# Kernel optimization log

Measured on AMD Instinct MI355X. Metric: run time of the kernel, lower is better.

## Reference

```python
import jax, jax.numpy as jnp
import numpy as np

N = 8192


def setup_inputs() -> dict:
    key = jax.random.key(0)
    ks = jax.random.split(key, 12)
    H_emb = jax.random.normal(ks[0], (645, 1140), jnp.float32) * 0.05
    H_emb = H_emb.at[0].set(0.0)  # padding_idx=0
    inp = {
        "ld_gcn": jax.random.normal(ks[1], (N, 512), jnp.float32),
        "ld_encoder": jax.random.normal(ks[2], (N, 512), jnp.float32),
        "x": jax.random.randint(ks[3], (N,), 0, 240),
        "y": jax.random.randint(ks[4], (N,), 0, 404),
        "H_emb": H_emb,
        "conv_w": jax.random.normal(ks[5], (32, 1, 2, 25), jnp.float32) * (1.0 / np.sqrt(2 * 25)),
        "conv_b": jnp.zeros((32,), jnp.float32),
        "W1": jax.random.normal(ks[6], (1000, 3968), jnp.float32) * (1.0 / np.sqrt(3968)),
        "b1": jnp.zeros((1000,), jnp.float32),
        "W2": jax.random.normal(ks[7], (100, 1000), jnp.float32) * (1.0 / np.sqrt(1000)),
        "b2": jnp.zeros((100,), jnp.float32),
        "Wg": jax.random.normal(ks[8], (100, 512), jnp.float32) * (1.0 / np.sqrt(512)),
        "bg": jnp.zeros((100,), jnp.float32),
        "We": jax.random.normal(ks[9], (100, 512), jnp.float32) * (1.0 / np.sqrt(512)),
        "be": jnp.zeros((100,), jnp.float32),
    }
    return inp


def reference(ld_gcn, ld_encoder, x, y, H_emb, conv_w, conv_b, W1, b1, W2, b2, Wg, bg, We, be):
    n = x.shape[0]
    lrelu = lambda t: jax.nn.leaky_relu(t, 0.01)
    # embedding lookups + concat -> (n,1,2,1140)
    h = jnp.concatenate([H_emb[x], H_emb[y + 240]], axis=1).reshape(n, 1, 2, 1140)
    # CNN: conv (2,25) stride (1,9) valid -> (n,32,1,124)
    c = jax.lax.conv_general_dilated(h, conv_w, window_strides=(1, 9), padding="VALID",
                                     dimension_numbers=("NCHW", "OIHW", "NCHW"))
    c = lrelu(c + conv_b[None, :, None, None]).reshape(n, -1)  # (n,3968)
    # fc_H (dropout = identity at eval)
    hfc = lrelu(c @ W1.T + b1)
    hfc = lrelu(hfc @ W2.T + b2)  # (n,100)
    # gating projections
    g = jnp.tanh(ld_gcn @ Wg.T + bg)       # (n,100)
    e = jnp.tanh(ld_encoder @ We.T + be)   # (n,100)
    # diagonal of (n,100)@(100,n) == row-wise dot product
    a_gcn = jnp.einsum("nd,nd->n", g, hfc)
    a_enc = jnp.einsum("nd,nd->n", e, hfc)
    att = jax.nn.softmax(jnp.stack([a_gcn, a_enc], axis=1), axis=1)  # (n,2)
    return ld_gcn * att[:, :1], ld_encoder * att[:, 1:]
```

## Files before the change

### kernel.cpp

```cpp
#include <hip/hip_runtime.h>
#include <hip/hip_bf16.h>

typedef unsigned short u16;
typedef short bf16x8 __attribute__((ext_vector_type(8)));
typedef float f32x4 __attribute__((ext_vector_type(4)));

#define NROWS 8192
#define EMBD  1140
#define FDIM  3968
#define N1R   1000
#define N1P   1024
#define N2R   100
#define N2P   128
#define DG    512

__device__ inline u16 f2b(float f) {
  __hip_bfloat16 h = __float2bfloat16(f);
  return *reinterpret_cast<u16*>(&h);
}

__device__ inline float b2f(u16 u) {
  unsigned v = (unsigned)u << 16;
  union { unsigned u; float f; } c;
  c.u = v;
  return c.f;
}

__device__ inline float tanh_fast(float x) {
  float ax = fabsf(x);
  float t = __expf(-2.f * ax);
  float r = (1.f - t) / (1.f + t);
  return x < 0.f ? -r : r;
}

__device__ inline void gld16(const void* g, void* l) {
  __builtin_amdgcn_global_load_lds(
      (const __attribute__((address_space(1))) unsigned int*)g,
      (__attribute__((address_space(3))) unsigned int*)l, 16, 0, 0);
}

__global__ __launch_bounds__(256) void prep_kernel(
    const float* __restrict__ W1, const float* __restrict__ W2,
    const float* __restrict__ Wg, const float* __restrict__ We,
    const float* __restrict__ H_emb, const float* __restrict__ conv_w,
    const float* __restrict__ conv_b,
    u16* __restrict__ W1bf, u16* __restrict__ W2bf,
    u16* __restrict__ Wgbf, u16* __restrict__ Webf,
    u16* __restrict__ Abuf, u16* __restrict__ Bbuf) {
  const int b = blockIdx.x;
  const int t = threadIdx.x;
  if (b < 2112) {
    const float* src;
    u16* dst;
    int row, c8, realRow, realCol;
    if (b < 1984) {
      int id = b * 256 + t;
      row = id / 496; c8 = (id - row * 496) * 8;
      src = W1 + (size_t)row * FDIM + c8;
      dst = W1bf + (size_t)row * FDIM + c8;
      realRow = N1R; realCol = FDIM;
    } else if (b < 2048) {
      int id = (b - 1984) * 256 + t;
      row = id >> 7; c8 = (id & 127) * 8;
      src = W2 + (size_t)row * N1R + c8;
      dst = W2bf + (size_t)row * N1P + c8;
      realRow = N2R; realCol = N1R;
    } else if (b < 2080) {
      int id = (b - 2048) * 256 + t;
      row = id >> 6; c8 = (id & 63) * 8;
      src = Wg + (size_t)row * DG + c8;
      dst = Wgbf + (size_t)row * DG + c8;
      realRow = N2R; realCol = DG;
    } else {
      int id = (b - 2080) * 256 + t;
      row = id >> 6; c8 = (id & 63) * 8;
      src = We + (size_t)row * DG + c8;
      dst = Webf + (size_t)row * DG + c8;
      realRow = N2R; realCol = DG;
    }
    bf16x8 o = (bf16x8){0, 0, 0, 0, 0, 0, 0, 0};
    if (row < realRow && c8 < realCol) {
#pragma unroll
      for (int j = 0; j < 8; ++j) o[j] = (short)f2b(src[j]);
    }
    *(bf16x8*)dst = o;
    return;
  }
  __shared__ float se[EMBD];
  __shared__ float sw[32 * 25];
  __shared__ float sb[32];
  const int eb = b - 2112;
  bool isA = eb < 240;
  const float* emb = H_emb + (size_t)eb * EMBD;
  u16* outp = isA ? (Abuf + (size_t)eb * FDIM) : (Bbuf + (size_t)(eb - 240) * FDIM);
  for (int i = t; i < EMBD; i += 256) se[i] = emb[i];
  int kh = isA ? 0 : 1;
  for (int i = t; i < 800; i += 256) {
    int o = i / 25, kw = i - o * 25;
    sw[i] = conv_w[o * 50 + kh * 25 + kw];
  }
  if (t < 32) sb[t] = isA ? conv_b[t] : 0.f;
  __syncthreads();
  for (int f = t; f < FDIM; f += 256) {
    int o = f / 124, wpos = f - o * 124;
    const float* e = se + wpos * 9;
    const float* wp = sw + o * 25;
    float acc = sb[o];
#pragma unroll
    for (int kw = 0; kw < 25; ++kw) acc += wp[kw] * e[kw];
    outp[f] = f2b(acc);
  }
}

__global__ __launch_bounds__(256) void conv_combine_kernel(
    const u16* __restrict__ Abuf, const u16* __restrict__ Bbuf,
    const int* __restrict__ xi, const int* __restrict__ yi, u16* __restrict__ cbf) {
  int r = blockIdx.x;
  const bf16x8* pa = (const bf16x8*)(Abuf + (size_t)xi[r] * FDIM);
  const bf16x8* pb = (const bf16x8*)(Bbuf + (size_t)yi[r] * FDIM);
  bf16x8* out = (bf16x8*)(cbf + (size_t)r * FDIM);
  for (int i = threadIdx.x; i < FDIM / 8; i += 256) {
    bf16x8 a = pa[i], b = pb[i];
    bf16x8 o;
#pragma unroll
    for (int j = 0; j < 8; ++j) {
      float v = b2f((u16)a[j]) + b2f((u16)b[j]);
      v = v > 0.f ? v : 0.01f * v;
      o[j] = (short)f2b(v);
    }
    out[i] = o;
  }
}

__global__ __launch_bounds__(256) void fc1_kernel(
    const u16* __restrict__ A, const u16* __restrict__ B,
    const float* __restrict__ bias, int realN,
    u16* __restrict__ C, int K, int ldc, int nTilesX) {
  const int nwg = gridDim.x;
  const int cpx = nwg >> 3;
  const int bid = blockIdx.x;
  const int wg = (bid & 7) * cpx + (bid >> 3);
  const int tm = (wg / nTilesX) * 128;
  const int tn = (wg % nTilesX) * 128;

  __shared__ u16 As[2][8192];
  __shared__ u16 Bs[2][8192];
  const int t = threadIdx.x;
  const int lane = t & 63;
  const int w = t >> 6;
  const int wr = (w >> 1) * 64, wc = (w & 1) * 64;
  const int fr = lane & 15;
  const int kg = lane >> 4;

  const int srow = lane >> 3;
  const int su = ((lane & 7) ^ srow) * 8;
  const u16* gA[4];
  const u16* gB[4];
  int ldsOff[4];
#pragma unroll
  for (int i = 0; i < 4; ++i) {
    const int c = w + i * 4;
    gA[i] = A + (size_t)(tm + c * 8 + srow) * K + su;
    gB[i] = B + (size_t)(tn + c * 8 + srow) * K + su;
    ldsOff[i] = c * 512;
  }

  f32x4 acc[4][4];
#pragma unroll
  for (int m = 0; m < 4; ++m)
#pragma unroll
    for (int n = 0; n < 4; ++n) acc[m][n] = (f32x4){0.f, 0.f, 0.f, 0.f};

  const int nk = K >> 6;
#pragma unroll
  for (int i = 0; i < 4; ++i) {
    gld16(gA[i], &As[0][ldsOff[i]]);
    gld16(gB[i], &Bs[0][ldsOff[i]]);
  }
  __syncthreads();

  for (int kt = 0; kt < nk; ++kt) {
    const int cb = kt & 1;
    if (kt + 1 < nk) {
      const int ko = (kt + 1) << 6;
#pragma unroll
      for (int i = 0; i < 4; ++i) {
        gld16(gA[i] + ko, &As[cb ^ 1][ldsOff[i]]);
        gld16(gB[i] + ko, &Bs[cb ^ 1][ldsOff[i]]);
      }
    }
    __builtin_amdgcn_sched_barrier(0);
#pragma unroll
    for (int ks = 0; ks < 2; ++ks) {
      const int un = ((ks * 4 + kg) ^ (fr & 7)) << 4;
      bf16x8 af[4], bff[4];
#pragma unroll
      for (int m = 0; m < 4; ++m)
        af[m] = *(const bf16x8*)((const char*)As[cb] + (wr + m * 16 + fr) * 128 + un);
#pragma unroll
      for (int n = 0; n < 4; ++n)
        bff[n] = *(const bf16x8*)((const char*)Bs[cb] + (wc + n * 16 + fr) * 128 + un);
#pragma unroll
      for (int m = 0; m < 4; ++m)
#pragma unroll
        for (int n = 0; n < 4; ++n)
          acc[m][n] = __builtin_amdgcn_mfma_f32_16x16x32_bf16(af[m], bff[n], acc[m][n], 0, 0, 0);
    }
    __syncthreads();
  }

#pragma unroll
  for (int n = 0; n < 4; ++n) {
    int col = tn + wc + n * 16 + fr;
    float bv = (col < realN) ? bias[col] : 0.f;
#pragma unroll
    for (int m = 0; m < 4; ++m) {
#pragma unroll
      for (int j = 0; j < 4; ++j) {
        int row = tm + wr + m * 16 + kg * 4 + j;
        float v = acc[m][n][j] + bv;
        v = v > 0.f ? v : 0.01f * v;
        C[(size_t)row * ldc + col] = f2b(v);
      }
    }
  }
}

__global__ __launch_bounds__(256) void tail_kernel(
    const u16* __restrict__ hfc1, const u16* __restrict__ W2bf, const float* __restrict__ b2,
    const float* __restrict__ ldg, const float* __restrict__ lde,
    const u16* __restrict__ Wgbf, const float* __restrict__ bg,
    const u16* __restrict__ Webf, const float* __restrict__ be,
    float* __restrict__ out0, float* __restrict__ out1) {
  __shared__ float H16[N2P][16];
  __shared__ float dpart[2][4][16];
  __shared__ float wt[2][16];

  const int tm = blockIdx.x * 16;
  const int t = threadIdx.x;
  const int lane = t & 63;
  const int w = t >> 6;
  const int fr = lane & 15;
  const int kg = lane >> 4;
  const int n0 = w * 2;

  {
    f32x4 a0e = (f32x4){0.f, 0.f, 0.f, 0.f}, a0o = a0e, a1e = a0e, a1o = a0e;
    const u16* Ap = hfc1 + (size_t)(tm + fr) * N1P + kg * 8;
    const u16* B0 = W2bf + (size_t)(n0 * 16 + fr) * N1P + kg * 8;
    const u16* B1 = B0 + (size_t)16 * N1P;
#pragma unroll 4
    for (int k2 = 0; k2 < 16; ++k2) {
      bf16x8 afe = *(const bf16x8*)(Ap + k2 * 64);
      bf16x8 afo = *(const bf16x8*)(Ap + k2 * 64 + 32);
      bf16x8 f0e = *(const bf16x8*)(B0 + k2 * 64);
      bf16x8 f0o = *(const bf16x8*)(B0 + k2 * 64 + 32);
      bf16x8 f1e = *(const bf16x8*)(B1 + k2 * 64);
      bf16x8 f1o = *(const bf16x8*)(B1 + k2 * 64 + 32);
      a0e = __builtin_amdgcn_mfma_f32_16x16x32_bf16(afe, f0e, a0e, 0, 0, 0);
      a1e = __builtin_amdgcn_mfma_f32_16x16x32_bf16(afe, f1e, a1e, 0, 0, 0);
      a0o = __builtin_amdgcn_mfma_f32_16x16x32_bf16(afo, f0o, a0o, 0, 0, 0);
      a1o = __builtin_amdgcn_mfma_f32_16x16x32_bf16(afo, f1o, a1o, 0, 0, 0);
    }
#pragma unroll
    for (int n = 0; n < 2; ++n) {
      int col = (n0 + n) * 16 + fr;
      float bv = (col < N2R) ? b2[col] : 0.f;
      f32x4 o;
#pragma unroll
      for (int j = 0; j < 4; ++j) {
        float x = (n == 0 ? a0e[j] + a0o[j] : a1e[j] + a1o[j]) + bv;
        o[j] = x > 0.f ? x : 0.01f * x;
      }
      *(f32x4*)&H16[col][kg * 4] = o;
    }
  }
  __syncthreads();

#pragma unroll 1
  for (int sec = 0; sec < 2; ++sec) {
    const float* ld = sec == 0 ? ldg : lde;
    const u16* Wb = sec == 0 ? Wgbf : Webf;
    const float* bb = sec == 0 ? bg : be;

    f32x4 a0e = (f32x4){0.f, 0.f, 0.f, 0.f}, a0o = a0e, a1e = a0e, a1o = a0e;
    const float* Ap = ld + (size_t)(tm + fr) * DG + kg * 8;
    const u16* B0 = Wb + (size_t)(n0 * 16 + fr) * DG + kg * 8;
    const u16* B1 = B0 + (size_t)16 * DG;
#pragma unroll 2
    for (int k2 = 0; k2 < 8; ++k2) {
      float4 v0 = *(const float4*)(Ap + k2 * 64);
      float4 v1 = *(const float4*)(Ap + k2 * 64 + 4);
      float4 v2 = *(const float4*)(Ap + k2 * 64 + 32);
      float4 v3 = *(const float4*)(Ap + k2 * 64 + 36);
      bf16x8 afe, afo;
      afe[0] = (short)f2b(v0.x); afe[1] = (short)f2b(v0.y);
      afe[2] = (short)f2b(v0.z); afe[3] = (short)f2b(v0.w);
      afe[4] = (short)f2b(v1.x); afe[5] = (short)f2b(v1.y);
      afe[6] = (short)f2b(v1.z); afe[7] = (short)f2b(v1.w);
      afo[0] = (short)f2b(v2.x); afo[1] = (short)f2b(v2.y);
      afo[2] = (short)f2b(v2.z); afo[3] = (short)f2b(v2.w);
      afo[4] = (short)f2b(v3.x); afo[5] = (short)f2b(v3.y);
      afo[6] = (short)f2b(v3.z); afo[7] = (short)f2b(v3.w);
      bf16x8 f0e = *(const bf16x8*)(B0 + k2 * 64);
      bf16x8 f0o = *(const bf16x8*)(B0 + k2 * 64 + 32);
      bf16x8 f1e = *(const bf16x8*)(B1 + k2 * 64);
      bf16x8 f1o = *(const bf16x8*)(B1 + k2 * 64 + 32);
      a0e = __builtin_amdgcn_mfma_f32_16x16x32_bf16(afe, f0e, a0e, 0, 0, 0);
      a1e = __builtin_amdgcn_mfma_f32_16x16x32_bf16(afe, f1e, a1e, 0, 0, 0);
      a0o = __builtin_amdgcn_mfma_f32_16x16x32_bf16(afo, f0o, a0o, 0, 0, 0);
      a1o = __builtin_amdgcn_mfma_f32_16x16x32_bf16(afo, f1o, a1o, 0, 0, 0);
    }
    float dv[4] = {0.f, 0.f, 0.f, 0.f};
#pragma unroll
    for (int n = 0; n < 2; ++n) {
      int col = (n0 + n) * 16 + fr;
      float bv = (col < N2R) ? bb[col] : 0.f;
      f32x4 h = *(const f32x4*)&H16[col][kg * 4];
#pragma unroll
      for (int j = 0; j < 4; ++j) {
        float s = (n == 0 ? a0e[j] + a0o[j] : a1e[j] + a1o[j]) + bv;
        dv[j] += tanh_fast(s) * h[j];
      }
    }
#pragma unroll
    for (int j = 0; j < 4; ++j) {
      float v = dv[j];
      v += __shfl_xor(v, 1);
      v += __shfl_xor(v, 2);
      v += __shfl_xor(v, 4);
      v += __shfl_xor(v, 8);
      dv[j] = v;
    }
    if (fr == 0) {
#pragma unroll
      for (int j = 0; j < 4; ++j) dpart[sec][w][kg * 4 + j] = dv[j];
    }
  }
  __syncthreads();

  if (t < 16) {
    float ag = dpart[0][0][t] + dpart[0][1][t] + dpart[0][2][t] + dpart[0][3][t];
    float ae = dpart[1][0][t] + dpart[1][1][t] + dpart[1][2][t] + dpart[1][3][t];
    float mm = fmaxf(ag, ae);
    float eg = __expf(ag - mm), eo = __expf(ae - mm);
    float inv = 1.f / (eg + eo);
    wt[0][t] = eg * inv;
    wt[1][t] = eo * inv;
  }
  __syncthreads();

  for (int i = t; i < 16 * (DG / 4); i += 256) {
    int r = i >> 7, c = i & 127;
    float w0 = wt[0][r], w1 = wt[1][r];
    size_t off = (size_t)(tm + r) * DG + c * 4;
    float4 a = *(const float4*)(ldg + off);
    a.x *= w0; a.y *= w0; a.z *= w0; a.w *= w0;
    *(float4*)(out0 + off) = a;
    float4 b = *(const float4*)(lde + off);
    b.x *= w1; b.y *= w1; b.z *= w1; b.w *= w1;
    *(float4*)(out1 + off) = b;
  }
}

extern "C" void kernel_launch(void* const* d_in, const int* in_sizes, int n_in,
                              void* d_out, int out_size, void* d_ws, size_t ws_size,
                              hipStream_t stream) {
  const float* ld_gcn = (const float*)d_in[0];
  const float* ld_enc = (const float*)d_in[1];
  const int*   xi     = (const int*)d_in[2];
  const int*   yi     = (const int*)d_in[3];
  const float* H_emb  = (const float*)d_in[4];
  const float* conv_w = (const float*)d_in[5];
  const float* conv_b = (const float*)d_in[6];
  const float* W1     = (const float*)d_in[7];
  const float* b1     = (const float*)d_in[8];
  const float* W2     = (const float*)d_in[9];
  const float* b2     = (const float*)d_in[10];
  const float* Wg     = (const float*)d_in[11];
  const float* bg     = (const float*)d_in[12];
  const float* We     = (const float*)d_in[13];
  const float* be     = (const float*)d_in[14];

  char* ws = (char*)d_ws;
  size_t off = 0;
  auto alloc = [&](size_t bytes) -> void* {
    void* p = ws + off;
    off = (off + bytes + 255) & ~(size_t)255;
    return p;
  };
  u16* Abuf = (u16*)alloc(240ull * FDIM * 2);
  u16* Bbuf = (u16*)alloc(404ull * FDIM * 2);
  u16* cbf  = (u16*)alloc((size_t)NROWS * FDIM * 2);
  u16* W1bf = (u16*)alloc((size_t)N1P * FDIM * 2);
  u16* W2bf = (u16*)alloc((size_t)N2P * N1P * 2);
  u16* Wgbf = (u16*)alloc((size_t)N2P * DG * 2);
  u16* Webf = (u16*)alloc((size_t)N2P * DG * 2);
  u16* hfc1 = (u16*)alloc((size_t)NROWS * N1P * 2);
  if (ws_size < off) return;

  prep_kernel<<<2756, 256, 0, stream>>>(W1, W2, Wg, We, H_emb, conv_w, conv_b,
                                        W1bf, W2bf, Wgbf, Webf, Abuf, Bbuf);
  conv_combine_kernel<<<NROWS, 256, 0, stream>>>(Abuf, Bbuf, xi, yi, cbf);

  fc1_kernel<<<dim3((NROWS / 128) * (N1P / 128)), 256, 0, stream>>>(
      cbf, W1bf, b1, N1R, hfc1, FDIM, N1P, N1P / 128);

  float* out0 = (float*)d_out;
  float* out1 = out0 + (size_t)NROWS * DG;
  tail_kernel<<<NROWS / 16, 256, 0, stream>>>(
      hfc1, W2bf, b2, ld_gcn, ld_enc, Wgbf, bg, Webf, be, out0, out1);
}
```

Baseline: 184.2 us.

## Move gating projections into gather kernel and precompute tanh outputs

```diff
diff --git a/kernel.cpp b/kernel.cpp
--- a/kernel.cpp
+++ b/kernel.cpp
@@ -33,6 +33,15 @@
   return x < 0.f ? -r : r;
 }
 
+__device__ inline bf16x8 cvt8(float4 a, float4 b) {
+  bf16x8 o;
+  o[0] = (short)f2b(a.x); o[1] = (short)f2b(a.y);
+  o[2] = (short)f2b(a.z); o[3] = (short)f2b(a.w);
+  o[4] = (short)f2b(b.x); o[5] = (short)f2b(b.y);
+  o[6] = (short)f2b(b.z); o[7] = (short)f2b(b.w);
+  return o;
+}
+
 __device__ inline void gld16(const void* g, void* l) {
   __builtin_amdgcn_global_load_lds(
       (const __attribute__((address_space(1))) unsigned int*)g,
@@ -41,15 +50,13 @@
 
 __global__ __launch_bounds__(256) void prep_kernel(
     const float* __restrict__ W1, const float* __restrict__ W2,
-    const float* __restrict__ Wg, const float* __restrict__ We,
     const float* __restrict__ H_emb, const float* __restrict__ conv_w,
     const float* __restrict__ conv_b,
     u16* __restrict__ W1bf, u16* __restrict__ W2bf,
-    u16* __restrict__ Wgbf, u16* __restrict__ Webf,
     u16* __restrict__ Abuf, u16* __restrict__ Bbuf) {
   const int b = blockIdx.x;
   const int t = threadIdx.x;
-  if (b < 2112) {
+  if (b < 2048) {
     const float* src;
     u16* dst;
     int row, c8, realRow, realCol;
@@ -59,24 +66,12 @@
       src = W1 + (size_t)row * FDIM + c8;
       dst = W1bf + (size_t)row * FDIM + c8;
       realRow = N1R; realCol = FDIM;
-    } else if (b < 2048) {
+    } else {
       int id = (b - 1984) * 256 + t;
       row = id >> 7; c8 = (id & 127) * 8;
       src = W2 + (size_t)row * N1R + c8;
       dst = W2bf + (size_t)row * N1P + c8;
       realRow = N2R; realCol = N1R;
-    } else if (b < 2080) {
-      int id = (b - 2048) * 256 + t;
-      row = id >> 6; c8 = (id & 63) * 8;
-      src = Wg + (size_t)row * DG + c8;
-      dst = Wgbf + (size_t)row * DG + c8;
-      realRow = N2R; realCol = DG;
-    } else {
-      int id = (b - 2080) * 256 + t;
-      row = id >> 6; c8 = (id & 63) * 8;
-      src = We + (size_t)row * DG + c8;
-      dst = Webf + (size_t)row * DG + c8;
-      realRow = N2R; realCol = DG;
     }
     bf16x8 o = (bf16x8){0, 0, 0, 0, 0, 0, 0, 0};
     if (row < realRow && c8 < realCol) {
@@ -89,7 +84,7 @@
   __shared__ float se[EMBD];
   __shared__ float sw[32 * 25];
   __shared__ float sb[32];
-  const int eb = b - 2112;
+  const int eb = b - 2048;
   bool isA = eb < 240;
   const float* emb = H_emb + (size_t)eb * EMBD;
   u16* outp = isA ? (Abuf + (size_t)eb * FDIM) : (Bbuf + (size_t)(eb - 240) * FDIM);
@@ -112,23 +107,91 @@
   }
 }
 
-__global__ __launch_bounds__(256) void conv_combine_kernel(
+__global__ __launch_bounds__(256) void cc_kernel(
     const u16* __restrict__ Abuf, const u16* __restrict__ Bbuf,
-    const int* __restrict__ xi, const int* __restrict__ yi, u16* __restrict__ cbf) {
-  int r = blockIdx.x;
-  const bf16x8* pa = (const bf16x8*)(Abuf + (size_t)xi[r] * FDIM);
-  const bf16x8* pb = (const bf16x8*)(Bbuf + (size_t)yi[r] * FDIM);
-  bf16x8* out = (bf16x8*)(cbf + (size_t)r * FDIM);
-  for (int i = threadIdx.x; i < FDIM / 8; i += 256) {
-    bf16x8 a = pa[i], b = pb[i];
-    bf16x8 o;
-#pragma unroll
-    for (int j = 0; j < 8; ++j) {
-      float v = b2f((u16)a[j]) + b2f((u16)b[j]);
-      v = v > 0.f ? v : 0.01f * v;
-      o[j] = (short)f2b(v);
-    }
-    out[i] = o;
+    const int* __restrict__ xi, const int* __restrict__ yi, u16* __restrict__ cbf,
+    const float* __restrict__ ldg, const float* __restrict__ lde,
+    const float* __restrict__ Wg, const float* __restrict__ We,
+    const float* __restrict__ bg, const float* __restrict__ be,
+    float* __restrict__ G, float* __restrict__ E) {
+  const int b = blockIdx.x;
+  const int t = threadIdx.x;
+  if (b < NROWS) {
+    const bf16x8* pa = (const bf16x8*)(Abuf + (size_t)xi[b] * FDIM);
+    const bf16x8* pb = (const bf16x8*)(Bbuf + (size_t)yi[b] * FDIM);
+    bf16x8* out = (bf16x8*)(cbf + (size_t)b * FDIM);
+    for (int i = t; i < FDIM / 8; i += 256) {
+      bf16x8 a = pa[i], bb = pb[i];
+      bf16x8 o;
+#pragma unroll
+      for (int j = 0; j < 8; ++j) {
+        float v = b2f((u16)a[j]) + b2f((u16)bb[j]);
+        v = v > 0.f ? v : 0.01f * v;
+        o[j] = (short)f2b(v);
+      }
+      out[i] = o;
+    }
+    return;
+  }
+  __shared__ float sH[16][128];
+  const int eb = b - NROWS;
+  const int sec = eb >> 9;
+  const int tm = (eb & 511) * 16;
+  const float* ld = sec ? lde : ldg;
+  const float* Wraw = sec ? We : Wg;
+  const float* bb = sec ? be : bg;
+  float* Gout = sec ? E : G;
+
+  const int lane = t & 63;
+  const int w = t >> 6;
+  const int fr = lane & 15;
+  const int kg = lane >> 4;
+  const int n0 = w * 2;
+
+  f32x4 a0e = (f32x4){0.f, 0.f, 0.f, 0.f}, a0o = a0e, a1e = a0e, a1o = a0e;
+  const float* Ap = ld + (size_t)(tm + fr) * DG + kg * 8;
+  const int r0 = n0 * 16 + fr, r1 = r0 + 16;
+  const bool val0 = r0 < N2R, val1 = r1 < N2R;
+  const float* W0 = Wraw + (size_t)(val0 ? r0 : 0) * DG + kg * 8;
+  const float* W1p = Wraw + (size_t)(val1 ? r1 : 0) * DG + kg * 8;
+  const bf16x8 z8 = (bf16x8){0, 0, 0, 0, 0, 0, 0, 0};
+#pragma unroll 2
+  for (int k2 = 0; k2 < 8; ++k2) {
+    float4 v0 = *(const float4*)(Ap + k2 * 64);
+    float4 v1 = *(const float4*)(Ap + k2 * 64 + 4);
+    float4 v2 = *(const float4*)(Ap + k2 * 64 + 32);
+    float4 v3 = *(const float4*)(Ap + k2 * 64 + 36);
+    bf16x8 afe = cvt8(v0, v1), afo = cvt8(v2, v3);
+    bf16x8 f0e = z8, f0o = z8, f1e = z8, f1o = z8;
+    if (val0) {
+      f0e = cvt8(*(const float4*)(W0 + k2 * 64), *(const float4*)(W0 + k2 * 64 + 4));
+      f0o = cvt8(*(const float4*)(W0 + k2 * 64 + 32), *(const float4*)(W0 + k2 * 64 + 36));
+    }
+    if (val1) {
+      f1e = cvt8(*(const float4*)(W1p + k2 * 64), *(const float4*)(W1p + k2 * 64 + 4));
+      f1o = cvt8(*(const float4*)(W1p + k2 * 64 + 32), *(const float4*)(W1p + k2 * 64 + 36));
+    }
+    a0e = __builtin_amdgcn_mfma_f32_16x16x32_bf16(afe, f0e, a0e, 0, 0, 0);
+    a1e = __builtin_amdgcn_mfma_f32_16x16x32_bf16(afe, f1e, a1e, 0, 0, 0);
+    a0o = __builtin_amdgcn_mfma_f32_16x16x32_bf16(afo, f0o, a0o, 0, 0, 0);
+    a1o = __builtin_amdgcn_mfma_f32_16x16x32_bf16(afo, f1o, a1o, 0, 0, 0);
+  }
+#pragma unroll
+  for (int n = 0; n < 2; ++n) {
+    int col = (n0 + n) * 16 + fr;
+    float bv = (col < N2R) ? bb[col] : 0.f;
+#pragma unroll
+    for (int j = 0; j < 4; ++j) {
+      float s = (n == 0 ? a0e[j] + a0o[j] : a1e[j] + a1o[j]) + bv;
+      sH[kg * 4 + j][col] = tanh_fast(s);
+    }
+  }
+  __syncthreads();
+  {
+    int row = t >> 4, c0 = (t & 15) * 8;
+    float* dst = Gout + (size_t)(tm + row) * N2P + c0;
+    *(f32x4*)dst = *(const f32x4*)&sH[row][c0];
+    *(f32x4*)(dst + 4) = *(const f32x4*)&sH[row][c0 + 4];
   }
 }
 
@@ -228,12 +291,12 @@
 
 __global__ __launch_bounds__(256) void tail_kernel(
     const u16* __restrict__ hfc1, const u16* __restrict__ W2bf, const float* __restrict__ b2,
+    const float* __restrict__ G, const float* __restrict__ E,
     const float* __restrict__ ldg, const float* __restrict__ lde,
-    const u16* __restrict__ Wgbf, const float* __restrict__ bg,
-    const u16* __restrict__ Webf, const float* __restrict__ be,
     float* __restrict__ out0, float* __restrict__ out1) {
   __shared__ float H16[N2P][16];
-  __shared__ float dpart[2][4][16];
+  __shared__ float dsG[4][16];
+  __shared__ float dsE[4][16];
   __shared__ float wt[2][16];
 
   const int tm = blockIdx.x * 16;
@@ -277,71 +340,27 @@
   }
   __syncthreads();
 
-#pragma unroll 1
-  for (int sec = 0; sec < 2; ++sec) {
-    const float* ld = sec == 0 ? ldg : lde;
-    const u16* Wb = sec == 0 ? Wgbf : Webf;
-    const float* bb = sec == 0 ? bg : be;
-
-    f32x4 a0e = (f32x4){0.f, 0.f, 0.f, 0.f}, a0o = a0e, a1e = a0e, a1o = a0e;
-    const float* Ap = ld + (size_t)(tm + fr) * DG + kg * 8;
-    const u16* B0 = Wb + (size_t)(n0 * 16 + fr) * DG + kg * 8;
-    const u16* B1 = B0 + (size_t)16 * DG;
-#pragma unroll 2
-    for (int k2 = 0; k2 < 8; ++k2) {
-      float4 v0 = *(const float4*)(Ap + k2 * 64);
-      float4 v1 = *(const float4*)(Ap + k2 * 64 + 4);
-      float4 v2 = *(const float4*)(Ap + k2 * 64 + 32);
-      float4 v3 = *(const float4*)(Ap + k2 * 64 + 36);
-      bf16x8 afe, afo;
-      afe[0] = (short)f2b(v0.x); afe[1] = (short)f2b(v0.y);
-      afe[2] = (short)f2b(v0.z); afe[3] = (short)f2b(v0.w);
-      afe[4] = (short)f2b(v1.x); afe[5] = (short)f2b(v1.y);
-      afe[6] = (short)f2b(v1.z); afe[7] = (short)f2b(v1.w);
-      afo[0] = (short)f2b(v2.x); afo[1] = (short)f2b(v2.y);
-      afo[2] = (short)f2b(v2.z); afo[3] = (short)f2b(v2.w);
-      afo[4] = (short)f2b(v3.x); afo[5] = (short)f2b(v3.y);
-      afo[6] = (short)f2b(v3.z); afo[7] = (short)f2b(v3.w);
-      bf16x8 f0e = *(const bf16x8*)(B0 + k2 * 64);
-      bf16x8 f0o = *(const bf16x8*)(B0 + k2 * 64 + 32);
-      bf16x8 f1e = *(const bf16x8*)(B1 + k2 * 64);
-      bf16x8 f1o = *(const bf16x8*)(B1 + k2 * 64 + 32);
-      a0e = __builtin_amdgcn_mfma_f32_16x16x32_bf16(afe, f0e, a0e, 0, 0, 0);
-      a1e = __builtin_amdgcn_mfma_f32_16x16x32_bf16(afe, f1e, a1e, 0, 0, 0);
-      a0o = __builtin_amdgcn_mfma_f32_16x16x32_bf16(afo, f0o, a0o, 0, 0, 0);
-      a1o = __builtin_amdgcn_mfma_f32_16x16x32_bf16(afo, f1o, a1o, 0, 0, 0);
-    }
-    float dv[4] = {0.f, 0.f, 0.f, 0.f};
-#pragma unroll
-    for (int n = 0; n < 2; ++n) {
-      int col = (n0 + n) * 16 + fr;
-      float bv = (col < N2R) ? bb[col] : 0.f;
-      f32x4 h = *(const f32x4*)&H16[col][kg * 4];
-#pragma unroll
-      for (int j = 0; j < 4; ++j) {
-        float s = (n == 0 ? a0e[j] + a0o[j] : a1e[j] + a1o[j]) + bv;
-        dv[j] += tanh_fast(s) * h[j];
-      }
-    }
-#pragma unroll
-    for (int j = 0; j < 4; ++j) {
-      float v = dv[j];
-      v += __shfl_xor(v, 1);
-      v += __shfl_xor(v, 2);
-      v += __shfl_xor(v, 4);
-      v += __shfl_xor(v, 8);
-      dv[j] = v;
-    }
-    if (fr == 0) {
-#pragma unroll
-      for (int j = 0; j < 4; ++j) dpart[sec][w][kg * 4 + j] = dv[j];
-    }
+  {
+    const int drow = t & 15;
+    const int d0 = (t >> 4 & 15) * 8;
+    float pg = 0.f, pe = 0.f;
+    const float* Gp = G + (size_t)(tm + drow) * N2P + d0;
+    const float* Ep = E + (size_t)(tm + drow) * N2P + d0;
+#pragma unroll
+    for (int j = 0; j < 8; ++j) {
+      float h = H16[d0 + j][drow];
+      pg += Gp[j] * h;
+      pe += Ep[j] * h;
+    }
+    pg += __shfl_xor(pg, 16); pg += __shfl_xor(pg, 32);
+    pe += __shfl_xor(pe, 16); pe += __shfl_xor(pe, 32);
+    if (lane < 16) { dsG[w][lane] = pg; dsE[w][lane] = pe; }
   }
   __syncthreads();
 
   if (t < 16) {
-    float ag = dpart[0][0][t] + dpart[0][1][t] + dpart[0][2][t] + dpart[0][3][t];
-    float ae = dpart[1][0][t] + dpart[1][1][t] + dpart[1][2][t] + dpart[1][3][t];
+    float ag = dsG[0][t] + dsG[1][t] + dsG[2][t] + dsG[3][t];
+    float ae = dsE[0][t] + dsE[1][t] + dsE[2][t] + dsE[3][t];
     float mm = fmaxf(ag, ae);
     float eg = __expf(ag - mm), eo = __expf(ae - mm);
     float inv = 1.f / (eg + eo);
@@ -389,19 +408,20 @@
     off = (off + bytes + 255) & ~(size_t)255;
     return p;
   };
-  u16* Abuf = (u16*)alloc(240ull * FDIM * 2);
-  u16* Bbuf = (u16*)alloc(404ull * FDIM * 2);
-  u16* cbf  = (u16*)alloc((size_t)NROWS * FDIM * 2);
-  u16* W1bf = (u16*)alloc((size_t)N1P * FDIM * 2);
-  u16* W2bf = (u16*)alloc((size_t)N2P * N1P * 2);
-  u16* Wgbf = (u16*)alloc((size_t)N2P * DG * 2);
-  u16* Webf = (u16*)alloc((size_t)N2P * DG * 2);
-  u16* hfc1 = (u16*)alloc((size_t)NROWS * N1P * 2);
+  u16*   Abuf = (u16*)alloc(240ull * FDIM * 2);
+  u16*   Bbuf = (u16*)alloc(404ull * FDIM * 2);
+  u16*   cbf  = (u16*)alloc((size_t)NROWS * FDIM * 2);
+  u16*   W1bf = (u16*)alloc((size_t)N1P * FDIM * 2);
+  u16*   W2bf = (u16*)alloc((size_t)N2P * N1P * 2);
+  u16*   hfc1 = (u16*)alloc((size_t)NROWS * N1P * 2);
+  float* G    = (float*)alloc((size_t)NROWS * N2P * 4);
+  float* E    = (float*)alloc((size_t)NROWS * N2P * 4);
   if (ws_size < off) return;
 
-  prep_kernel<<<2756, 256, 0, stream>>>(W1, W2, Wg, We, H_emb, conv_w, conv_b,
-                                        W1bf, W2bf, Wgbf, Webf, Abuf, Bbuf);
-  conv_combine_kernel<<<NROWS, 256, 0, stream>>>(Abuf, Bbuf, xi, yi, cbf);
+  prep_kernel<<<2692, 256, 0, stream>>>(W1, W2, H_emb, conv_w, conv_b,
+                                        W1bf, W2bf, Abuf, Bbuf);
+  cc_kernel<<<NROWS + 1024, 256, 0, stream>>>(Abuf, Bbuf, xi, yi, cbf,
+                                              ld_gcn, ld_enc, Wg, We, bg, be, G, E);
 
   fc1_kernel<<<dim3((NROWS / 128) * (N1P / 128)), 256, 0, stream>>>(
       cbf, W1bf, b1, N1R, hfc1, FDIM, N1P, N1P / 128);
@@ -409,5 +429,5 @@
   float* out0 = (float*)d_out;
   float* out1 = out0 + (size_t)NROWS * DG;
   tail_kernel<<<NROWS / 16, 256, 0, stream>>>(
-      hfc1, W2bf, b2, ld_gcn, ld_enc, Wgbf, bg, Webf, be, out0, out1);
-}
+      hfc1, W2bf, b2, G, E, ld_gcn, ld_enc, out0, out1);
+}
```

Result: slower. 211.1 us (+14.6%).

## Split tail kernel K-loops across 16 waves with shared-memory partial reductions

Applied to the files above, without the earlier changes.

```diff
diff --git a/kernel.cpp b/kernel.cpp
--- a/kernel.cpp
+++ b/kernel.cpp
@@ -226,14 +226,17 @@
   }
 }
 
-__global__ __launch_bounds__(256) void tail_kernel(
+__global__ __launch_bounds__(1024) void tail_kernel(
     const u16* __restrict__ hfc1, const u16* __restrict__ W2bf, const float* __restrict__ b2,
     const float* __restrict__ ldg, const float* __restrict__ lde,
     const u16* __restrict__ Wgbf, const float* __restrict__ bg,
     const u16* __restrict__ Webf, const float* __restrict__ be,
     float* __restrict__ out0, float* __restrict__ out1) {
+  __shared__ float P2[4][N2P][16];
   __shared__ float H16[N2P][16];
-  __shared__ float dpart[2][4][16];
+  __shared__ float GT[2][N2P][16];
+  __shared__ float ds[2][16][16];
+  __shared__ float asum[2][16];
   __shared__ float wt[2][16];
 
   const int tm = blockIdx.x * 16;
@@ -242,21 +245,22 @@
   const int w = t >> 6;
   const int fr = lane & 15;
   const int kg = lane >> 4;
-  const int n0 = w * 2;
 
   {
+    const int kc = w >> 2;
+    const int n0 = (w & 3) * 2;
     f32x4 a0e = (f32x4){0.f, 0.f, 0.f, 0.f}, a0o = a0e, a1e = a0e, a1o = a0e;
-    const u16* Ap = hfc1 + (size_t)(tm + fr) * N1P + kg * 8;
-    const u16* B0 = W2bf + (size_t)(n0 * 16 + fr) * N1P + kg * 8;
+    const u16* Ap = hfc1 + (size_t)(tm + fr) * N1P + kc * 256 + kg * 8;
+    const u16* B0 = W2bf + (size_t)(n0 * 16 + fr) * N1P + kc * 256 + kg * 8;
     const u16* B1 = B0 + (size_t)16 * N1P;
-#pragma unroll 4
-    for (int k2 = 0; k2 < 16; ++k2) {
-      bf16x8 afe = *(const bf16x8*)(Ap + k2 * 64);
-      bf16x8 afo = *(const bf16x8*)(Ap + k2 * 64 + 32);
-      bf16x8 f0e = *(const bf16x8*)(B0 + k2 * 64);
-      bf16x8 f0o = *(const bf16x8*)(B0 + k2 * 64 + 32);
-      bf16x8 f1e = *(const bf16x8*)(B1 + k2 * 64);
-      bf16x8 f1o = *(const bf16x8*)(B1 + k2 * 64 + 32);
+#pragma unroll
+    for (int i = 0; i < 4; ++i) {
+      bf16x8 afe = *(const bf16x8*)(Ap + i * 64);
+      bf16x8 afo = *(const bf16x8*)(Ap + i * 64 + 32);
+      bf16x8 f0e = *(const bf16x8*)(B0 + i * 64);
+      bf16x8 f0o = *(const bf16x8*)(B0 + i * 64 + 32);
+      bf16x8 f1e = *(const bf16x8*)(B1 + i * 64);
+      bf16x8 f1o = *(const bf16x8*)(B1 + i * 64 + 32);
       a0e = __builtin_amdgcn_mfma_f32_16x16x32_bf16(afe, f0e, a0e, 0, 0, 0);
       a1e = __builtin_amdgcn_mfma_f32_16x16x32_bf16(afe, f1e, a1e, 0, 0, 0);
       a0o = __builtin_amdgcn_mfma_f32_16x16x32_bf16(afo, f0o, a0o, 0, 0, 0);
@@ -265,34 +269,37 @@
 #pragma unroll
     for (int n = 0; n < 2; ++n) {
       int col = (n0 + n) * 16 + fr;
-      float bv = (col < N2R) ? b2[col] : 0.f;
-      f32x4 o;
-#pragma unroll
-      for (int j = 0; j < 4; ++j) {
-        float x = (n == 0 ? a0e[j] + a0o[j] : a1e[j] + a1o[j]) + bv;
-        o[j] = x > 0.f ? x : 0.01f * x;
-      }
-      *(f32x4*)&H16[col][kg * 4] = o;
-    }
-  }
-  __syncthreads();
-
-#pragma unroll 1
-  for (int sec = 0; sec < 2; ++sec) {
-    const float* ld = sec == 0 ? ldg : lde;
-    const u16* Wb = sec == 0 ? Wgbf : Webf;
-    const float* bb = sec == 0 ? bg : be;
-
+#pragma unroll
+      for (int j = 0; j < 4; ++j)
+        P2[kc][col][kg * 4 + j] = (n == 0 ? a0e[j] + a0o[j] : a1e[j] + a1o[j]);
+    }
+  }
+  __syncthreads();
+
+  for (int e = t; e < N2P * 16; e += 1024) {
+    int col = e >> 4, row = e & 15;
+    float s = P2[0][col][row] + P2[1][col][row] + P2[2][col][row] + P2[3][col][row];
+    s += (col < N2R) ? b2[col] : 0.f;
+    H16[col][row] = s > 0.f ? s : 0.01f * s;
+  }
+  __syncthreads();
+
+  {
+    const int sec = w >> 3;
+    const int kc2 = (w & 7) >> 2;
+    const int n0 = (w & 3) * 2;
+    const float* ld = sec ? lde : ldg;
+    const u16* Wb = sec ? Webf : Wgbf;
     f32x4 a0e = (f32x4){0.f, 0.f, 0.f, 0.f}, a0o = a0e, a1e = a0e, a1o = a0e;
-    const float* Ap = ld + (size_t)(tm + fr) * DG + kg * 8;
-    const u16* B0 = Wb + (size_t)(n0 * 16 + fr) * DG + kg * 8;
+    const float* Ap = ld + (size_t)(tm + fr) * DG + kc2 * 256 + kg * 8;
+    const u16* B0 = Wb + (size_t)(n0 * 16 + fr) * DG + kc2 * 256 + kg * 8;
     const u16* B1 = B0 + (size_t)16 * DG;
-#pragma unroll 2
-    for (int k2 = 0; k2 < 8; ++k2) {
-      float4 v0 = *(const float4*)(Ap + k2 * 64);
-      float4 v1 = *(const float4*)(Ap + k2 * 64 + 4);
-      float4 v2 = *(const float4*)(Ap + k2 * 64 + 32);
-      float4 v3 = *(const float4*)(Ap + k2 * 64 + 36);
+#pragma unroll
+    for (int i = 0; i < 4; ++i) {
+      float4 v0 = *(const float4*)(Ap + i * 64);
+      float4 v1 = *(const float4*)(Ap + i * 64 + 4);
+      float4 v2 = *(const float4*)(Ap + i * 64 + 32);
+      float4 v3 = *(const float4*)(Ap + i * 64 + 36);
       bf16x8 afe, afo;
       afe[0] = (short)f2b(v0.x); afe[1] = (short)f2b(v0.y);
       afe[2] = (short)f2b(v0.z); afe[3] = (short)f2b(v0.w);
@@ -302,46 +309,53 @@
       afo[2] = (short)f2b(v2.z); afo[3] = (short)f2b(v2.w);
       afo[4] = (short)f2b(v3.x); afo[5] = (short)f2b(v3.y);
       afo[6] = (short)f2b(v3.z); afo[7] = (short)f2b(v3.w);
-      bf16x8 f0e = *(const bf16x8*)(B0 + k2 * 64);
-      bf16x8 f0o = *(const bf16x8*)(B0 + k2 * 64 + 32);
-      bf16x8 f1e = *(const bf16x8*)(B1 + k2 * 64);
-      bf16x8 f1o = *(const bf16x8*)(B1 + k2 * 64 + 32);
+      bf16x8 f0e = *(const bf16x8*)(B0 + i * 64);
+      bf16x8 f0o = *(const bf16x8*)(B0 + i * 64 + 32);
+      bf16x8 f1e = *(const bf16x8*)(B1 + i * 64);
+      bf16x8 f1o = *(const bf16x8*)(B1 + i * 64 + 32);
       a0e = __builtin_amdgcn_mfma_f32_16x16x32_bf16(afe, f0e, a0e, 0, 0, 0);
       a1e = __builtin_amdgcn_mfma_f32_16x16x32_bf16(afe, f1e, a1e, 0, 0, 0);
       a0o = __builtin_amdgcn_mfma_f32_16x16x32_bf16(afo, f0o, a0o, 0, 0, 0);
       a1o = __builtin_amdgcn_mfma_f32_16x16x32_bf16(afo, f1o, a1o, 0, 0, 0);
     }
-    float dv[4] = {0.f, 0.f, 0.f, 0.f};
 #pragma unroll
     for (int n = 0; n < 2; ++n) {
       int col = (n0 + n) * 16 + fr;
-      float bv = (col < N2R) ? bb[col] : 0.f;
-      f32x4 h = *(const f32x4*)&H16[col][kg * 4];
-#pragma unroll
-      for (int j = 0; j < 4; ++j) {
-        float s = (n == 0 ? a0e[j] + a0o[j] : a1e[j] + a1o[j]) + bv;
-        dv[j] += tanh_fast(s) * h[j];
-      }
-    }
-#pragma unroll
-    for (int j = 0; j < 4; ++j) {
-      float v = dv[j];
-      v += __shfl_xor(v, 1);
-      v += __shfl_xor(v, 2);
-      v += __shfl_xor(v, 4);
-      v += __shfl_xor(v, 8);
-      dv[j] = v;
-    }
-    if (fr == 0) {
-#pragma unroll
-      for (int j = 0; j < 4; ++j) dpart[sec][w][kg * 4 + j] = dv[j];
-    }
+#pragma unroll
+      for (int j = 0; j < 4; ++j)
+        P2[sec * 2 + kc2][col][kg * 4 + j] = (n == 0 ? a0e[j] + a0o[j] : a1e[j] + a1o[j]);
+    }
+  }
+  __syncthreads();
+
+  for (int e = t; e < 2 * N2P * 16; e += 1024) {
+    int sec = e >> 11;
+    int col = (e >> 4) & 127, row = e & 15;
+    float s = P2[sec * 2][col][row] + P2[sec * 2 + 1][col][row];
+    s += (col < N2R) ? (sec ? be[col] : bg[col]) : 0.f;
+    GT[sec][col][row] = tanh_fast(s) * H16[col][row];
+  }
+  __syncthreads();
+
+  if (t < 512) {
+    int sec = t >> 8, row = (t >> 4) & 15, ch = t & 15;
+    float s = 0.f;
+#pragma unroll
+    for (int j = 0; j < 8; ++j) s += GT[sec][ch * 8 + j][row];
+    ds[sec][row][ch] = s;
+  }
+  __syncthreads();
+  if (t < 32) {
+    int sec = t >> 4, row = t & 15;
+    float s = 0.f;
+#pragma unroll
+    for (int j = 0; j < 16; ++j) s += ds[sec][row][j];
+    asum[sec][row] = s;
   }
   __syncthreads();
 
   if (t < 16) {
-    float ag = dpart[0][0][t] + dpart[0][1][t] + dpart[0][2][t] + dpart[0][3][t];
-    float ae = dpart[1][0][t] + dpart[1][1][t] + dpart[1][2][t] + dpart[1][3][t];
+    float ag = asum[0][t], ae = asum[1][t];
     float mm = fmaxf(ag, ae);
     float eg = __expf(ag - mm), eo = __expf(ae - mm);
     float inv = 1.f / (eg + eo);
@@ -350,7 +364,7 @@
   }
   __syncthreads();
 
-  for (int i = t; i < 16 * (DG / 4); i += 256) {
+  for (int i = t; i < 16 * (DG / 4); i += 1024) {
     int r = i >> 7, c = i & 127;
     float w0 = wt[0][r], w1 = wt[1][r];
     size_t off = (size_t)(tm + r) * DG + c * 4;
@@ -408,6 +422,6 @@
 
   float* out0 = (float*)d_out;
   float* out1 = out0 + (size_t)NROWS * DG;
-  tail_kernel<<<NROWS / 16, 256, 0, stream>>>(
+  tail_kernel<<<NROWS / 16, 1024, 0, stream>>>(
       hfc1, W2bf, b2, ld_gcn, ld_enc, Wgbf, bg, Webf, be, out0, out1);
 }
```

Result: no change. 185.8 us (+0.9%).

## Fuse all stages into one cooperative persistent kernel with grid syncs

Applied to the files above, without the earlier changes.

```diff
diff --git a/kernel.cpp b/kernel.cpp
--- a/kernel.cpp
+++ b/kernel.cpp
@@ -1,5 +1,8 @@
 #include <hip/hip_runtime.h>
 #include <hip/hip_bf16.h>
+#include <hip/hip_cooperative_groups.h>
+
+namespace cg = cooperative_groups;
 
 typedef unsigned short u16;
 typedef short bf16x8 __attribute__((ext_vector_type(8)));
@@ -39,7 +42,8 @@
       (__attribute__((address_space(3))) unsigned int*)l, 16, 0, 0);
 }
 
-__global__ __launch_bounds__(256) void prep_kernel(
+
+__device__ void prep_body(int b, int t, char* smem,
     const float* __restrict__ W1, const float* __restrict__ W2,
     const float* __restrict__ Wg, const float* __restrict__ We,
     const float* __restrict__ H_emb, const float* __restrict__ conv_w,
@@ -47,8 +51,6 @@
     u16* __restrict__ W1bf, u16* __restrict__ W2bf,
     u16* __restrict__ Wgbf, u16* __restrict__ Webf,
     u16* __restrict__ Abuf, u16* __restrict__ Bbuf) {
-  const int b = blockIdx.x;
-  const int t = threadIdx.x;
   if (b < 2112) {
     const float* src;
     u16* dst;
@@ -86,9 +88,9 @@
     *(bf16x8*)dst = o;
     return;
   }
-  __shared__ float se[EMBD];
-  __shared__ float sw[32 * 25];
-  __shared__ float sb[32];
+  float* se = (float*)smem;
+  float* sw = se + 1152;
+  float* sb = sw + 800;
   const int eb = b - 2112;
   bool isA = eb < 240;
   const float* emb = H_emb + (size_t)eb * EMBD;
@@ -112,14 +114,13 @@
   }
 }
 
-__global__ __launch_bounds__(256) void conv_combine_kernel(
+__device__ void cc_body(int r, int t,
     const u16* __restrict__ Abuf, const u16* __restrict__ Bbuf,
     const int* __restrict__ xi, const int* __restrict__ yi, u16* __restrict__ cbf) {
-  int r = blockIdx.x;
   const bf16x8* pa = (const bf16x8*)(Abuf + (size_t)xi[r] * FDIM);
   const bf16x8* pb = (const bf16x8*)(Bbuf + (size_t)yi[r] * FDIM);
   bf16x8* out = (bf16x8*)(cbf + (size_t)r * FDIM);
-  for (int i = threadIdx.x; i < FDIM / 8; i += 256) {
+  for (int i = t; i < FDIM / 8; i += 256) {
     bf16x8 a = pa[i], b = pb[i];
     bf16x8 o;
 #pragma unroll
@@ -132,20 +133,16 @@
   }
 }
 
-__global__ __launch_bounds__(256) void fc1_kernel(
+__device__ void fc1_body(int vb, int t, char* smem,
     const u16* __restrict__ A, const u16* __restrict__ B,
-    const float* __restrict__ bias, int realN,
-    u16* __restrict__ C, int K, int ldc, int nTilesX) {
-  const int nwg = gridDim.x;
-  const int cpx = nwg >> 3;
-  const int bid = blockIdx.x;
-  const int wg = (bid & 7) * cpx + (bid >> 3);
-  const int tm = (wg / nTilesX) * 128;
-  const int tn = (wg % nTilesX) * 128;
-
-  __shared__ u16 As[2][8192];
-  __shared__ u16 Bs[2][8192];
-  const int t = threadIdx.x;
+    const float* __restrict__ bias, u16* __restrict__ C) {
+  u16* AsP = (u16*)smem;
+  u16* BsP = AsP + 16384;
+  const int wg = (vb & 7) * 64 + (vb >> 3);
+  const int tm = (wg / 8) * 128;
+  const int tn = (wg % 8) * 128;
+  const int K = FDIM;
+
   const int lane = t & 63;
   const int w = t >> 6;
   const int wr = (w >> 1) * 64, wc = (w & 1) * 64;
@@ -174,8 +171,8 @@
   const int nk = K >> 6;
 #pragma unroll
   for (int i = 0; i < 4; ++i) {
-    gld16(gA[i], &As[0][ldsOff[i]]);
-    gld16(gB[i], &Bs[0][ldsOff[i]]);
+    gld16(gA[i], AsP + ldsOff[i]);
+    gld16(gB[i], BsP + ldsOff[i]);
   }
   __syncthreads();
 
@@ -185,8 +182,8 @@
       const int ko = (kt + 1) << 6;
 #pragma unroll
       for (int i = 0; i < 4; ++i) {
-        gld16(gA[i] + ko, &As[cb ^ 1][ldsOff[i]]);
-        gld16(gB[i] + ko, &Bs[cb ^ 1][ldsOff[i]]);
+        gld16(gA[i] + ko, AsP + (cb ^ 1) * 8192 + ldsOff[i]);
+        gld16(gB[i] + ko, BsP + (cb ^ 1) * 8192 + ldsOff[i]);
       }
     }
     __builtin_amdgcn_sched_barrier(0);
@@ -196,10 +193,10 @@
       bf16x8 af[4], bff[4];
 #pragma unroll
       for (int m = 0; m < 4; ++m)
-        af[m] = *(const bf16x8*)((const char*)As[cb] + (wr + m * 16 + fr) * 128 + un);
+        af[m] = *(const bf16x8*)((const char*)(AsP + cb * 8192) + (wr + m * 16 + fr) * 128 + un);
 #pragma unroll
       for (int n = 0; n < 4; ++n)
-        bff[n] = *(const bf16x8*)((const char*)Bs[cb] + (wc + n * 16 + fr) * 128 + un);
+        bff[n] = *(const bf16x8*)((const char*)(BsP + cb * 8192) + (wc + n * 16 + fr) * 128 + un);
 #pragma unroll
       for (int m = 0; m < 4; ++m)
 #pragma unroll
@@ -212,7 +209,7 @@
 #pragma unroll
   for (int n = 0; n < 4; ++n) {
     int col = tn + wc + n * 16 + fr;
-    float bv = (col < realN) ? bias[col] : 0.f;
+    float bv = (col < N1R) ? bias[col] : 0.f;
 #pragma unroll
     for (int m = 0; m < 4; ++m) {
 #pragma unroll
@@ -220,24 +217,23 @@
         int row = tm + wr + m * 16 + kg * 4 + j;
         float v = acc[m][n][j] + bv;
         v = v > 0.f ? v : 0.01f * v;
-        C[(size_t)row * ldc + col] = f2b(v);
+        C[(size_t)row * N1P + col] = f2b(v);
       }
     }
   }
 }
 
-__global__ __launch_bounds__(256) void tail_kernel(
+__device__ void tail_body(int vb, int t, char* smem,
     const u16* __restrict__ hfc1, const u16* __restrict__ W2bf, const float* __restrict__ b2,
     const float* __restrict__ ldg, const float* __restrict__ lde,
     const u16* __restrict__ Wgbf, const float* __restrict__ bg,
     const u16* __restrict__ Webf, const float* __restrict__ be,
     float* __restrict__ out0, float* __restrict__ out1) {
-  __shared__ float H16[N2P][16];
-  __shared__ float dpart[2][4][16];
-  __shared__ float wt[2][16];
-
-  const int tm = blockIdx.x * 16;
-  const int t = threadIdx.x;
+  float (*H16)[16] = (float(*)[16])smem;
+  float* dpart = (float*)(smem + 8192);
+  float* wt = (float*)(smem + 8704);
+
+  const int tm = vb * 16;
   const int lane = t & 63;
   const int w = t >> 6;
   const int fr = lane & 15;
@@ -334,25 +330,25 @@
     }
     if (fr == 0) {
 #pragma unroll
-      for (int j = 0; j < 4; ++j) dpart[sec][w][kg * 4 + j] = dv[j];
+      for (int j = 0; j < 4; ++j) dpart[(sec * 4 + w) * 16 + kg * 4 + j] = dv[j];
     }
   }
   __syncthreads();
 
   if (t < 16) {
-    float ag = dpart[0][0][t] + dpart[0][1][t] + dpart[0][2][t] + dpart[0][3][t];
-    float ae = dpart[1][0][t] + dpart[1][1][t] + dpart[1][2][t] + dpart[1][3][t];
+    float ag = dpart[0 + t] + dpart[16 + t] + dpart[32 + t] + dpart[48 + t];
+    float ae = dpart[64 + t] + dpart[80 + t] + dpart[96 + t] + dpart[112 + t];
     float mm = fmaxf(ag, ae);
     float eg = __expf(ag - mm), eo = __expf(ae - mm);
     float inv = 1.f / (eg + eo);
-    wt[0][t] = eg * inv;
-    wt[1][t] = eo * inv;
+    wt[t] = eg * inv;
+    wt[16 + t] = eo * inv;
   }
   __syncthreads();
 
   for (int i = t; i < 16 * (DG / 4); i += 256) {
     int r = i >> 7, c = i & 127;
-    float w0 = wt[0][r], w1 = wt[1][r];
+    float w0 = wt[r], w1 = wt[16 + r];
     size_t off = (size_t)(tm + r) * DG + c * 4;
     float4 a = *(const float4*)(ldg + off);
     a.x *= w0; a.y *= w0; a.z *= w0; a.w *= w0;
@@ -361,6 +357,93 @@
     b.x *= w1; b.y *= w1; b.z *= w1; b.w *= w1;
     *(float4*)(out1 + off) = b;
   }
+}
+
+__global__ __launch_bounds__(512) void mega_kernel(
+    const float* __restrict__ W1, const float* __restrict__ W2,
+    const float* __restrict__ Wg, const float* __restrict__ We,
+    const float* __restrict__ H_emb, const float* __restrict__ conv_w,
+    const float* __restrict__ conv_b,
+    u16* __restrict__ W1bf, u16* __restrict__ W2bf,
+    u16* __restrict__ Wgbf, u16* __restrict__ Webf,
+    u16* __restrict__ Abuf, u16* __restrict__ Bbuf,
+    const int* __restrict__ xi, const int* __restrict__ yi,
+    u16* __restrict__ cbf, const float* __restrict__ b1, u16* __restrict__ hfc1,
+    const float* __restrict__ ldg, const float* __restrict__ lde,
+    const float* __restrict__ b2, const float* __restrict__ bg,
+    const float* __restrict__ be,
+    float* __restrict__ out0, float* __restrict__ out1) {
+  extern __shared__ __align__(16) char smem_dyn[];
+  cg::grid_group grid = cg::this_grid();
+  const int t512 = threadIdx.x;
+  const int half = t512 >> 8;
+  const int t = t512 & 255;
+  const int bid = blockIdx.x;
+  char* smem = smem_dyn + half * 65536;
+
+  {
+    const int vb = bid * 2 + half;
+#pragma unroll 1
+    for (int it = 0; it < 6; ++it) {
+      int b = vb + it * 512;
+      if (b < 2756)
+        prep_body(b, t, smem, W1, W2, Wg, We, H_emb, conv_w, conv_b,
+                  W1bf, W2bf, Wgbf, Webf, Abuf, Bbuf);
+      __syncthreads();
+    }
+  }
+  grid.sync();
+
+  {
+    const int vb = bid * 2 + half;
+#pragma unroll 1
+    for (int r = vb; r < NROWS; r += 512)
+      cc_body(r, t, Abuf, Bbuf, xi, yi, cbf);
+  }
+  grid.sync();
+
+  fc1_body(bid + half * 256, t, smem, cbf, W1bf, b1, hfc1);
+  grid.sync();
+
+  tail_body(bid * 2 + half, t, smem, hfc1, W2bf, b2, ldg, lde,
+            Wgbf, bg, Webf, be, out0, out1);
+}
+
+__global__ __launch_bounds__(256) void prep_kernel(
+    const float* __restrict__ W1, const float* __restrict__ W2,
+    const float* __restrict__ Wg, const float* __restrict__ We,
+    const float* __restrict__ H_emb, const float* __restrict__ conv_w,
+    const float* __restrict__ conv_b,
+    u16* __restrict__ W1bf, u16* __restrict__ W2bf,
+    u16* __restrict__ Wgbf, u16* __restrict__ Webf,
+    u16* __restrict__ Abuf, u16* __restrict__ Bbuf) {
+  __shared__ __align__(16) char smem[8192];
+  prep_body(blockIdx.x, threadIdx.x, smem, W1, W2, Wg, We, H_emb, conv_w, conv_b,
+            W1bf, W2bf, Wgbf, Webf, Abuf, Bbuf);
+}
+
+__global__ __launch_bounds__(256) void conv_combine_kernel(
+    const u16* __restrict__ Abuf, const u16* __restrict__ Bbuf,
+    const int* __restrict__ xi, const int* __restrict__ yi, u16* __restrict__ cbf) {
+  cc_body(blockIdx.x, threadIdx.x, Abuf, Bbuf, xi, yi, cbf);
+}
+
+__global__ __launch_bounds__(256) void fc1_kernel(
+    const u16* __restrict__ A, const u16* __restrict__ B,
+    const float* __restrict__ bias, u16* __restrict__ C) {
+  __shared__ __align__(16) char smem[65536];
+  fc1_body(blockIdx.x, threadIdx.x, smem, A, B, bias, C);
+}
+
+__global__ __launch_bounds__(256) void tail_kernel(
+    const u16* __restrict__ hfc1, const u16* __restrict__ W2bf, const float* __restrict__ b2,
+    const float* __restrict__ ldg, const float* __restrict__ lde,
+    const u16* __restrict__ Wgbf, const float* __restrict__ bg,
+    const u16* __restrict__ Webf, const float* __restrict__ be,
+    float* __restrict__ out0, float* __restrict__ out1) {
+  __shared__ __align__(16) char smem[8704 + 128];
+  tail_body(blockIdx.x, threadIdx.x, smem, hfc1, W2bf, b2, ldg, lde,
+            Wgbf, bg, Webf, be, out0, out1);
 }
 
 extern "C" void kernel_launch(void* const* d_in, const int* in_sizes, int n_in,
@@ -399,15 +482,29 @@
   u16* hfc1 = (u16*)alloc((size_t)NROWS * N1P * 2);
   if (ws_size < off) return;
 
-  prep_kernel<<<2756, 256, 0, stream>>>(W1, W2, Wg, We, H_emb, conv_w, conv_b,
-                                        W1bf, W2bf, Wgbf, Webf, Abuf, Bbuf);
-  conv_combine_kernel<<<NROWS, 256, 0, stream>>>(Abuf, Bbuf, xi, yi, cbf);
-
-  fc1_kernel<<<dim3((NROWS / 128) * (N1P / 128)), 256, 0, stream>>>(
-      cbf, W1bf, b1, N1R, hfc1, FDIM, N1P, N1P / 128);
-
   float* out0 = (float*)d_out;
   float* out1 = out0 + (size_t)NROWS * DG;
-  tail_kernel<<<NROWS / 16, 256, 0, stream>>>(
-      hfc1, W2bf, b2, ld_gcn, ld_enc, Wgbf, bg, Webf, be, out0, out1);
-}
+
+  hipFuncSetAttribute((const void*)mega_kernel,
+                      hipFuncAttributeMaxDynamicSharedMemorySize, 131072);
+
+  void* args[] = {
+    (void*)&W1, (void*)&W2, (void*)&Wg, (void*)&We, (void*)&H_emb,
+    (void*)&conv_w, (void*)&conv_b,
+    (void*)&W1bf, (void*)&W2bf, (void*)&Wgbf, (void*)&Webf,
+    (void*)&Abuf, (void*)&Bbuf,
+    (void*)&xi, (void*)&yi, (void*)&cbf, (void*)&b1, (void*)&hfc1,
+    (void*)&ld_gcn, (void*)&ld_enc, (void*)&b2, (void*)&bg, (void*)&be,
+    (void*)&out0, (void*)&out1
+  };
+  hipError_t err = hipLaunchCooperativeKernel((void*)mega_kernel, dim3(256), dim3(512),
+                                              args, 131072, stream);
+  if (err != hipSuccess) {
+    prep_kernel<<<2756, 256, 0, stream>>>(W1, W2, Wg, We, H_emb, conv_w, conv_b,
+                                          W1bf, W2bf, Wgbf, Webf, Abuf, Bbuf);
+    conv_combine_kernel<<<NROWS, 256, 0, stream>>>(Abuf, Bbuf, xi, yi, cbf);
+    fc1_kernel<<<512, 256, 0, stream>>>(cbf, W1bf, b1, hfc1);
+    tail_kernel<<<512, 256, 0, stream>>>(hfc1, W2bf, b2, ld_gcn, ld_enc,
+                                         Wgbf, bg, Webf, be, out0, out1);
+  }
+}
```

Result: slower. 301.4 us (+63.6%).
